# Performance work log

Hardware: AMD Instinct MI355X
Metric: run time of the kernel (lower is better)

The kernel has to match this reference:

```python
import jax, jax.numpy as jnp
import numpy as np

ALPHAS = [0.1, 0.3, 0.5]
WEIGHTS = [0.5, 0.3, 0.2]


def setup_inputs() -> dict:
    key = jax.random.key(0)
    k1, k2 = jax.random.split(key)
    pred = jax.random.normal(k1, (64, 4096, 64), dtype=jnp.float32)
    target = jax.random.normal(k2, (64, 4096, 64), dtype=jnp.float32)
    return {"pred": pred, "target": target}


def _ema(x, alpha):
    # x: [B, T, D]; EMA along axis 1: y0 = x0, y_t = alpha*x_t + (1-alpha)*y_{t-1}
    x0 = x[:, 0]                      # [B, D]
    xs = jnp.moveaxis(x[:, 1:], 1, 0)  # [T-1, B, D] for scan over time

    def step(carry, xt):
        y = alpha * xt + (1.0 - alpha) * carry
        return y, y

    _, ys = jax.lax.scan(step, x0, xs)  # [T-1, B, D]
    return jnp.concatenate([x0[:, None], jnp.moveaxis(ys, 0, 1)], axis=1)


def reference(pred, target):
    loss = None
    for alpha, weight in zip(ALPHAS, WEIGHTS):
        pe = _ema(pred, alpha)
        te = _ema(target, alpha)
        mse = jnp.mean((pe - te) ** 2, axis=1)  # [B, D]
        term = weight * mse
        loss = term if loss is None else loss + term
    return jnp.mean(loss)  # reduction='mean'
```

## Files before the change

### kernel.cpp

```cpp
#include <hip/hip_runtime.h>


#define T_LEN 4096
#define F_LEN 64
#define NB    64
#define NPAIR 4096

constexpr double powd(double r, int n) {
    double v = 1.0, b = r;
    while (n > 0) { if (n & 1) v *= b; b *= b; n >>= 1; }
    return v;
}

template<int NCHUNK>
__global__ __launch_bounds__(64)
void mstl_pass1(const float4* __restrict__ pred,
                const float4* __restrict__ targ,
                float* __restrict__ ws)
{
    constexpr int CHUNK = T_LEN / NCHUNK;
    constexpr int NSTG  = CHUNK / 4;
    constexpr float R0 = 0.9f, R1 = 0.7f, R2 = 0.5f;
    constexpr float A0 = 0.1f, A1 = 0.3f, A2 = 0.5f;

    const int lane = threadIdx.x;
    const int g    = lane >> 4;
    const int fl   = lane & 15;
    const int task = blockIdx.x * 4 + g;
    const int b    = task / NCHUNK;
    const int c    = task % NCHUNK;

    const float4* __restrict__ p = pred + (size_t)(b * T_LEN + c * CHUNK) * 16 + fl;
    const float4* __restrict__ q = targ + (size_t)(b * T_LEN + c * CHUNK) * 16 + fl;

    float4 z0{0,0,0,0}, z1{0,0,0,0}, z2{0,0,0,0};
    float4 a0{0,0,0,0}, a1{0,0,0,0}, a2{0,0,0,0};
    float4 b0{0,0,0,0}, b1{0,0,0,0}, b2{0,0,0,0};
    float  w0 = R0, w1 = R1, w2 = R2;

    float4 pA0,pA1,pA2,pA3, qA0,qA1,qA2,qA3;
    float4 pB0,pB1,pB2,pB3, qB0,qB1,qB2,qB3;

#define LOADA(t0) { pA0=p[(size_t)(t0)*16];     pA1=p[(size_t)((t0)+1)*16]; \
                    pA2=p[(size_t)((t0)+2)*16]; pA3=p[(size_t)((t0)+3)*16]; \
                    qA0=q[(size_t)(t0)*16];     qA1=q[(size_t)((t0)+1)*16]; \
                    qA2=q[(size_t)((t0)+2)*16]; qA3=q[(size_t)((t0)+3)*16]; }
#define LOADB(t0) { pB0=p[(size_t)(t0)*16];     pB1=p[(size_t)((t0)+1)*16]; \
                    pB2=p[(size_t)((t0)+2)*16]; pB3=p[(size_t)((t0)+3)*16]; \
                    qB0=q[(size_t)(t0)*16];     qB1=q[(size_t)((t0)+1)*16]; \
                    qB2=q[(size_t)((t0)+2)*16]; qB3=q[(size_t)((t0)+3)*16]; }
#define STEP(P,Q) { \
    const float dx=(P).x-(Q).x, dy=(P).y-(Q).y, dz=(P).z-(Q).z, dw=(P).w-(Q).w; \
    z0.x=fmaf(R0,z0.x,A0*dx); a0.x=fmaf(z0.x,z0.x,a0.x); b0.x=fmaf(z0.x,w0,b0.x); \
    z0.y=fmaf(R0,z0.y,A0*dy); a0.y=fmaf(z0.y,z0.y,a0.y); b0.y=fmaf(z0.y,w0,b0.y); \
    z0.z=fmaf(R0,z0.z,A0*dz); a0.z=fmaf(z0.z,z0.z,a0.z); b0.z=fmaf(z0.z,w0,b0.z); \
    z0.w=fmaf(R0,z0.w,A0*dw); a0.w=fmaf(z0.w,z0.w,a0.w); b0.w=fmaf(z0.w,w0,b0.w); \
    w0 *= R0; \
    z1.x=fmaf(R1,z1.x,A1*dx); a1.x=fmaf(z1.x,z1.x,a1.x); b1.x=fmaf(z1.x,w1,b1.x); \
    z1.y=fmaf(R1,z1.y,A1*dy); a1.y=fmaf(z1.y,z1.y,a1.y); b1.y=fmaf(z1.y,w1,b1.y); \
    z1.z=fmaf(R1,z1.z,A1*dz); a1.z=fmaf(z1.z,z1.z,a1.z); b1.z=fmaf(z1.z,w1,b1.z); \
    z1.w=fmaf(R1,z1.w,A1*dw); a1.w=fmaf(z1.w,z1.w,a1.w); b1.w=fmaf(z1.w,w1,b1.w); \
    w1 *= R1; \
    z2.x=fmaf(R2,z2.x,A2*dx); a2.x=fmaf(z2.x,z2.x,a2.x); b2.x=fmaf(z2.x,w2,b2.x); \
    z2.y=fmaf(R2,z2.y,A2*dy); a2.y=fmaf(z2.y,z2.y,a2.y); b2.y=fmaf(z2.y,w2,b2.y); \
    z2.z=fmaf(R2,z2.z,A2*dz); a2.z=fmaf(z2.z,z2.z,a2.z); b2.z=fmaf(z2.z,w2,b2.z); \
    z2.w=fmaf(R2,z2.w,A2*dw); a2.w=fmaf(z2.w,z2.w,a2.w); b2.w=fmaf(z2.w,w2,b2.w); \
    w2 *= R2; }
#define COMPA() { STEP(pA0,qA0) STEP(pA1,qA1) STEP(pA2,qA2) STEP(pA3,qA3) }
#define COMPB() { STEP(pB0,qB0) STEP(pB1,qB1) STEP(pB2,qB2) STEP(pB3,qB3) }

    LOADA(0);
    #pragma unroll
    for (int s = 0; s < NSTG; s += 2) {
        LOADB((s + 1) * 4);
        COMPA();
        if (s + 2 < NSTG) LOADA((s + 2) * 4);
        COMPB();
    }
#undef LOADA
#undef LOADB
#undef STEP
#undef COMPA
#undef COMPB

    const int pf = b * F_LEN + fl * 4;
#define ST(slot, val) *(float4*)(ws + ((size_t)(slot) * NCHUNK + c) * NPAIR + pf) = (val);
    ST(0, a0) ST(1, b0) ST(2, z0)
    ST(3, a1) ST(4, b1) ST(5, z1)
    ST(6, a2) ST(7, b2) ST(8, z2)
#undef ST
}

template<int NCHUNK>
__global__ __launch_bounds__(64)
void mstl_pass2(const float* __restrict__ ws,
                const float* __restrict__ pred,
                const float* __restrict__ targ,
                float* __restrict__ out)
{
    constexpr int CHUNK = T_LEN / NCHUNK;
    constexpr float RL[3] = { (float)powd(0.9, CHUNK), (float)powd(0.7, CHUNK),
                              (float)powd(0.5, CHUNK) };
    constexpr float CC[3] = {
        (float)(0.81 * (1.0 - powd(0.9, 2*CHUNK)) / (1.0 - 0.81)),
        (float)(0.49 * (1.0 - powd(0.7, 2*CHUNK)) / (1.0 - 0.49)),
        (float)(0.25 * (1.0 - powd(0.5, 2*CHUNK)) / (1.0 - 0.25)) };
    constexpr float WGT[3] = { 0.5f, 0.3f, 0.2f };

    const int a   = blockIdx.x >> 6;
    const int pfb = blockIdx.x & 63;
    const int pf  = pfb * 64 + threadIdx.x;
    const int b   = pf >> 6, f = pf & 63;

    const float rl = (a == 0) ? RL[0] : (a == 1) ? RL[1] : RL[2];
    const float cc = (a == 0) ? CC[0] : (a == 1) ? CC[1] : CC[2];
    const float wg = (a == 0) ? WGT[0] : (a == 1) ? WGT[1] : WGT[2];

    const size_t row0 = (size_t)b * T_LEN * F_LEN + f;
    float e = pred[row0] - targ[row0];

    const float* __restrict__ base = ws + (size_t)(a * 3) * NCHUNK * NPAIR + pf;

    float s = 0.f;
    #pragma unroll 16
    for (int c = 0; c < NCHUNK; ++c) {
        float A = base[((size_t)0 * NCHUNK + c) * NPAIR];
        float B = base[((size_t)1 * NCHUNK + c) * NPAIR];
        float Z = base[((size_t)2 * NCHUNK + c) * NPAIR];
        s += A + e * (2.f * B + e * cc);
        e = fmaf(rl, e, Z);
    }

    float total = s * wg;
    #pragma unroll
    for (int off = 32; off > 0; off >>= 1)
        total += __shfl_down(total, off, 64);

    if (threadIdx.x == 0)
        atomicAdd(out, total * (1.0f / 16777216.0f));
}

extern "C" void kernel_launch(void* const* d_in, const int* in_sizes, int n_in,
                              void* d_out, int out_size, void* d_ws, size_t ws_size,
                              hipStream_t stream) {
    const float* pred = (const float*)d_in[0];
    const float* targ = (const float*)d_in[1];
    float* out = (float*)d_out;
    float* ws  = (float*)d_ws;

    hipMemsetAsync(out, 0, sizeof(float) * out_size, stream);

    const size_t need64 = (size_t)9 * 64 * NPAIR * sizeof(float);
    if (ws_size >= need64) {
        mstl_pass1<64><<<dim3(NB * 64 / 4), dim3(64), 0, stream>>>(
            (const float4*)pred, (const float4*)targ, ws);
        mstl_pass2<64><<<dim3(192), dim3(64), 0, stream>>>(ws, pred, targ, out);
    } else {
        mstl_pass1<32><<<dim3(NB * 32 / 4), dim3(64), 0, stream>>>(
            (const float4*)pred, (const float4*)targ, ws);
        mstl_pass2<32><<<dim3(192), dim3(64), 0, stream>>>(ws, pred, targ, out);
    }
}
```

Measured before the change: 166.4 us.

## Add hierarchical segment combine pass and raise chunk count for more parallelism

Splits the serial cross-chunk combine into a parallel per-segment pass (pass2a) that folds groups of chunks into segment-level partial sums, followed by a short serial pass over 16 segments. This lets the time axis be cut into up to 256 chunks, so pass1 launches many more blocks and each has a shorter serial scan. The cost is a third kernel launch, an extra workspace round trip, and more workspace traffic from storing more chunk partials.

```diff
diff --git a/kernel.cpp b/kernel.cpp
--- a/kernel.cpp
+++ b/kernel.cpp
@@ -5,12 +5,15 @@
 #define F_LEN 64
 #define NB    64
 #define NPAIR 4096
+#define SEGS  16
 
 constexpr double powd(double r, int n) {
     double v = 1.0, b = r;
     while (n > 0) { if (n & 1) v *= b; b *= b; n >>= 1; }
     return v;
 }
+constexpr double RAD[3] = {0.9, 0.7, 0.5};
+constexpr float  WGT[3] = {0.5f, 0.3f, 0.2f};
 
 template<int NCHUNK>
 __global__ __launch_bounds__(64)
@@ -93,51 +96,109 @@
 
 template<int NCHUNK>
 __global__ __launch_bounds__(64)
-void mstl_pass2(const float* __restrict__ ws,
-                const float* __restrict__ pred,
-                const float* __restrict__ targ,
-                float* __restrict__ out)
+void mstl_pass2a(const float* __restrict__ ws, float* __restrict__ ws2)
 {
+    constexpr int CPS   = NCHUNK / SEGS;
     constexpr int CHUNK = T_LEN / NCHUNK;
-    constexpr float RL[3] = { (float)powd(0.9, CHUNK), (float)powd(0.7, CHUNK),
-                              (float)powd(0.5, CHUNK) };
-    constexpr float CC[3] = {
-        (float)(0.81 * (1.0 - powd(0.9, 2*CHUNK)) / (1.0 - 0.81)),
-        (float)(0.49 * (1.0 - powd(0.7, 2*CHUNK)) / (1.0 - 0.49)),
-        (float)(0.25 * (1.0 - powd(0.5, 2*CHUNK)) / (1.0 - 0.25)) };
-    constexpr float WGT[3] = { 0.5f, 0.3f, 0.2f };
+    constexpr float RLv[3] = { (float)powd(RAD[0], CHUNK), (float)powd(RAD[1], CHUNK),
+                               (float)powd(RAD[2], CHUNK) };
+    constexpr float CAv[3] = {
+        (float)(RAD[0]*RAD[0] * (1.0 - powd(RAD[0], 2*CHUNK)) / (1.0 - RAD[0]*RAD[0])),
+        (float)(RAD[1]*RAD[1] * (1.0 - powd(RAD[1], 2*CHUNK)) / (1.0 - RAD[1]*RAD[1])),
+        (float)(RAD[2]*RAD[2] * (1.0 - powd(RAD[2], 2*CHUNK)) / (1.0 - RAD[2]*RAD[2])) };
+
+    const int bid = blockIdx.x;
+    const int a   = bid >> 10;
+    const int rem = bid & 1023;
+    const int s   = rem >> 6;
+    const int pfb = rem & 63;
+    const int pf  = pfb * 64 + threadIdx.x;
+
+    const float rl = (a == 0) ? RLv[0] : (a == 1) ? RLv[1] : RLv[2];
+    const float cA = (a == 0) ? CAv[0] : (a == 1) ? CAv[1] : CAv[2];
+
+    const float* __restrict__ base = ws + (size_t)(a * 3) * NCHUNK * NPAIR + pf;
+
+    float u = 0.f, Ap = 0.f, Bp = 0.f, w = 1.f;
+    #pragma unroll
+    for (int c = 0; c < CPS; ++c) {
+        const int gc = s * CPS + c;
+        float A = base[((size_t)0 * NCHUNK + gc) * NPAIR];
+        float B = base[((size_t)1 * NCHUNK + gc) * NPAIR];
+        float Z = base[((size_t)2 * NCHUNK + gc) * NPAIR];
+        Ap += A + u * (2.f * B + cA * u);
+        Bp += w * (B + cA * u);
+        u   = fmaf(rl, u, Z);
+        w  *= rl;
+    }
+
+    float* o = ws2 + ((size_t)(a * SEGS + s) * 3) * NPAIR + pf;
+    o[(size_t)0 * NPAIR] = Ap;
+    o[(size_t)1 * NPAIR] = Bp;
+    o[(size_t)2 * NPAIR] = u;
+}
+
+template<int NCHUNK>
+__global__ __launch_bounds__(64)
+void mstl_pass2b(const float* __restrict__ ws2,
+                 const float* __restrict__ pred,
+                 const float* __restrict__ targ,
+                 float* __restrict__ out)
+{
+    constexpr int CPS   = NCHUNK / SEGS;
+    constexpr int CHUNK = T_LEN / NCHUNK;
+    constexpr float RLS[3] = { (float)powd(RAD[0], CHUNK*CPS), (float)powd(RAD[1], CHUNK*CPS),
+                               (float)powd(RAD[2], CHUNK*CPS) };
+    constexpr double rl2_0 = powd(RAD[0], 2*CHUNK), rl2_1 = powd(RAD[1], 2*CHUNK),
+                     rl2_2 = powd(RAD[2], 2*CHUNK);
+    constexpr float CP[3] = {
+        (float)((RAD[0]*RAD[0] * (1.0 - powd(RAD[0], 2*CHUNK)) / (1.0 - RAD[0]*RAD[0]))
+                * (1.0 - powd(rl2_0, CPS)) / (1.0 - rl2_0)),
+        (float)((RAD[1]*RAD[1] * (1.0 - powd(RAD[1], 2*CHUNK)) / (1.0 - RAD[1]*RAD[1]))
+                * (1.0 - powd(rl2_1, CPS)) / (1.0 - rl2_1)),
+        (float)((RAD[2]*RAD[2] * (1.0 - powd(RAD[2], 2*CHUNK)) / (1.0 - RAD[2]*RAD[2]))
+                * (1.0 - powd(rl2_2, CPS)) / (1.0 - rl2_2)) };
 
     const int a   = blockIdx.x >> 6;
     const int pfb = blockIdx.x & 63;
     const int pf  = pfb * 64 + threadIdx.x;
     const int b   = pf >> 6, f = pf & 63;
 
-    const float rl = (a == 0) ? RL[0] : (a == 1) ? RL[1] : RL[2];
-    const float cc = (a == 0) ? CC[0] : (a == 1) ? CC[1] : CC[2];
-    const float wg = (a == 0) ? WGT[0] : (a == 1) ? WGT[1] : WGT[2];
+    const float rls = (a == 0) ? RLS[0] : (a == 1) ? RLS[1] : RLS[2];
+    const float cp  = (a == 0) ? CP[0]  : (a == 1) ? CP[1]  : CP[2];
+    const float wg  = (a == 0) ? WGT[0] : (a == 1) ? WGT[1] : WGT[2];
 
     const size_t row0 = (size_t)b * T_LEN * F_LEN + f;
     float e = pred[row0] - targ[row0];
 
-    const float* __restrict__ base = ws + (size_t)(a * 3) * NCHUNK * NPAIR + pf;
-
-    float s = 0.f;
-    #pragma unroll 16
-    for (int c = 0; c < NCHUNK; ++c) {
-        float A = base[((size_t)0 * NCHUNK + c) * NPAIR];
-        float B = base[((size_t)1 * NCHUNK + c) * NPAIR];
-        float Z = base[((size_t)2 * NCHUNK + c) * NPAIR];
-        s += A + e * (2.f * B + e * cc);
-        e = fmaf(rl, e, Z);
+    float S = 0.f;
+    #pragma unroll
+    for (int s = 0; s < SEGS; ++s) {
+        const float* o = ws2 + ((size_t)(a * SEGS + s) * 3) * NPAIR + pf;
+        float Ap = o[(size_t)0 * NPAIR];
+        float Bp = o[(size_t)1 * NPAIR];
+        float Zp = o[(size_t)2 * NPAIR];
+        S += Ap + e * (2.f * Bp + cp * e);
+        e  = fmaf(rls, e, Zp);
     }
 
-    float total = s * wg;
+    float total = S * wg;
     #pragma unroll
     for (int off = 32; off > 0; off >>= 1)
         total += __shfl_down(total, off, 64);
 
     if (threadIdx.x == 0)
         atomicAdd(out, total * (1.0f / 16777216.0f));
+}
+
+template<int NCHUNK>
+static void launch_all(const float* pred, const float* targ,
+                       float* out, float* ws, hipStream_t stream) {
+    float* ws2 = ws + (size_t)9 * NCHUNK * NPAIR;
+    mstl_pass1<NCHUNK><<<dim3(NB * NCHUNK / 4), dim3(64), 0, stream>>>(
+        (const float4*)pred, (const float4*)targ, ws);
+    mstl_pass2a<NCHUNK><<<dim3(3 * SEGS * 64), dim3(64), 0, stream>>>(ws, ws2);
+    mstl_pass2b<NCHUNK><<<dim3(192), dim3(64), 0, stream>>>(ws2, pred, targ, out);
 }
 
 extern "C" void kernel_launch(void* const* d_in, const int* in_sizes, int n_in,
@@ -150,14 +211,11 @@
 
     hipMemsetAsync(out, 0, sizeof(float) * out_size, stream);
 
-    const size_t need64 = (size_t)9 * 64 * NPAIR * sizeof(float);
-    if (ws_size >= need64) {
-        mstl_pass1<64><<<dim3(NB * 64 / 4), dim3(64), 0, stream>>>(
-            (const float4*)pred, (const float4*)targ, ws);
-        mstl_pass2<64><<<dim3(192), dim3(64), 0, stream>>>(ws, pred, targ, out);
-    } else {
-        mstl_pass1<32><<<dim3(NB * 32 / 4), dim3(64), 0, stream>>>(
-            (const float4*)pred, (const float4*)targ, ws);
-        mstl_pass2<32><<<dim3(192), dim3(64), 0, stream>>>(ws, pred, targ, out);
-    }
-}
+    auto need = [](int nchunk) {
+        return (size_t)(9 * nchunk + 3 * SEGS * 3) * NPAIR * sizeof(float);
+    };
+    if      (ws_size >= need(256)) launch_all<256>(pred, targ, out, ws, stream);
+    else if (ws_size >= need(128)) launch_all<128>(pred, targ, out, ws, stream);
+    else if (ws_size >= need(64))  launch_all<64>(pred, targ, out, ws, stream);
+    else                           launch_all<32>(pred, targ, out, ws, stream);
+}
```

Measured after the change: 167.4 us. Within noise of the previous version (+0.6%).
